# Kernel optimization log

Hardware: AMD Instinct MI355X
Metric: run time of the kernel (lower is better)

Reference implementation:

```python
import jax, jax.numpy as jnp
import numpy as np

D_MODEL = 1024
NUM_HEADS = 16
DK = D_MODEL // NUM_HEADS
THETA = 10000.0
B, S = 4, 2048


def _rope(x, pos):
    # x: [B, H, S, dk], pos: [S] int positions
    half = DK // 2
    inv_freq = THETA ** (-jnp.arange(half, dtype=jnp.float32) * 2.0 / DK)  # [half]
    ang = pos.astype(jnp.float32)[:, None] * inv_freq[None, :]             # [S, half]
    cos, sin = jnp.cos(ang), jnp.sin(ang)                                  # [S, half]
    x_even = x[..., 0::2]
    x_odd = x[..., 1::2]
    out_even = x_even * cos - x_odd * sin
    out_odd = x_even * sin + x_odd * cos
    # interleave back to [..., dk]
    return jnp.stack([out_even, out_odd], axis=-1).reshape(x.shape)


def setup_inputs() -> dict:
    key = jax.random.key(0)
    ks = jax.random.split(key, 5)
    scale = 1.0 / np.sqrt(D_MODEL)
    return {
        "x": jax.random.normal(ks[0], (B, S, D_MODEL), dtype=jnp.float32),
        "token_position": jnp.arange(S, dtype=jnp.int32),
        "wq": jax.random.normal(ks[1], (D_MODEL, D_MODEL), dtype=jnp.float32) * scale,
        "wk": jax.random.normal(ks[2], (D_MODEL, D_MODEL), dtype=jnp.float32) * scale,
        "wv": jax.random.normal(ks[3], (D_MODEL, D_MODEL), dtype=jnp.float32) * scale,
        "wo": jax.random.normal(ks[4], (D_MODEL, D_MODEL), dtype=jnp.float32) * scale,
    }


def reference(x, token_position, wq, wk, wv, wo):
    b, s, _ = x.shape
    # QKV projections (torch Linear: y = x @ W.T), split heads -> [B, H, S, dk]
    def proj(w):
        y = jnp.einsum("bsd,ed->bse", x, w)
        return y.reshape(b, s, NUM_HEADS, DK).transpose(0, 2, 1, 3)
    q, k, v = proj(wq), proj(wk), proj(wv)
    q = _rope(q, token_position)
    k = _rope(k, token_position)
    # causal SDPA
    scores = jnp.einsum("bhqd,bhkd->bhqk", q, k) / jnp.sqrt(jnp.float32(DK))
    causal = jnp.tril(jnp.ones((s, s), dtype=bool))
    scores = jnp.where(causal, scores, -jnp.inf)
    attn = jax.nn.softmax(scores, axis=-1)
    out = jnp.einsum("bhqk,bhkd->bhqd", attn, v)          # [B, H, S, dv]
    out = out.transpose(0, 2, 1, 3).reshape(b, s, D_MODEL)  # merge heads
    return jnp.einsum("bsd,ed->bse", out, wo)             # output projection
```

## Files before the change

### kernel.cpp

```cpp
#include <hip/hip_runtime.h>


#define D_MODEL 1024
#define NH      16
#define DKH     64
#define SEQ     2048
#define BATCH   4
#define SCALE_LOG2 0.180336875461f
#define ROPE_L2    0.41524101186092029f

typedef _Float16 f16;
typedef _Float16 f16x8 __attribute__((ext_vector_type(8)));
typedef _Float16 f16x4 __attribute__((ext_vector_type(4)));
typedef __fp16   fp16x2n __attribute__((ext_vector_type(2)));
typedef float    f32x4 __attribute__((ext_vector_type(4)));
typedef unsigned short u16;
typedef unsigned int   u32;

__device__ __forceinline__ void glds16(const void* g, void* l) {
  __builtin_amdgcn_global_load_lds((const __attribute__((address_space(1))) void*)g,
                                   (__attribute__((address_space(3))) void*)l, 16, 0, 0);
}
__device__ __forceinline__ u32 pk(float a, float b) {
  union { fp16x2n h; u32 u; } c; c.h = __builtin_amdgcn_cvt_pkrtz(a, b); return c.u;
}

#define VMW_(N) asm volatile("s_waitcnt vmcnt(" #N ")" ::: "memory")
#define VMW(N) VMW_(N)
#define PRE_MFMA() do {                                                       \
    __builtin_amdgcn_s_barrier();                                             \
    asm volatile("s_waitcnt lgkmcnt(0)" ::: "memory");                        \
    __builtin_amdgcn_sched_barrier(0);                                        \
  } while (0)

__global__ void cvt_all(const float* __restrict__ x,
                        const float* __restrict__ w0, const float* __restrict__ w1,
                        const float* __restrict__ w2, const float* __restrict__ w3,
                        f16* __restrict__ xo, f16* __restrict__ o0, f16* __restrict__ o1,
                        f16* __restrict__ o2, f16* __restrict__ o3) {
  int blk = blockIdx.x;
  const float* src; f16* dst; int off;
  if (blk < 8192) { src = x; dst = xo; off = blk; }
  else {
    int t = blk - 8192; int w = t >> 10; off = t & 1023;
    switch (w) { case 0: src = w0; dst = o0; break;  case 1: src = w1; dst = o1; break;
                 case 2: src = w2; dst = o2; break;  default: src = w3; dst = o3; break; }
  }
  int i = (off * 256 + threadIdx.x) * 4;
  float4 v = *(const float4*)(src + i);
  uint2 o; o.x = pk(v.x, v.y); o.y = pk(v.z, v.w);
  *(uint2*)(dst + i) = o;
}

__global__ __launch_bounds__(512, 2) void gemm_qkv(const f16* __restrict__ A,
                                                   const f16* __restrict__ W,
                                                   f16* __restrict__ Qo,
                                                   f16* __restrict__ Ko,
                                                   f16* __restrict__ Vo,
                                                   const int* __restrict__ pos) {
  extern __shared__ char lds[];
  const int bid  = blockIdx.x;
  const int lin  = (bid & 7) * 64 + (bid >> 3);
  const int bx   = lin & 15, by = lin >> 4;
  const int m0   = by * 256, n0 = bx * 192;
  const int tid  = threadIdx.x;
  const int wave = tid >> 6, lane = tid & 63;
  const int quad = lane >> 4, l16 = lane & 15;
  const int wr   = wave >> 2, wc = wave & 3;

  f32x4 acc[8][3];
#pragma unroll
  for (int i = 0; i < 8; ++i)
#pragma unroll
    for (int j = 0; j < 3; ++j) acc[i][j] = (f32x4){0.f, 0.f, 0.f, 0.f};

  const int posR = (l16 & 1) * 4 + (quad ^ ((l16 >> 1) & 3));
  const char* aRd  = lds + wr * 8192 + (l16 >> 1) * 128 + posR * 16;
  const char* bRd0 = lds + 65536 + (wc * 48 + l16) * 128 + ((quad) ^ (l16 & 7)) * 16;
  const char* bRd1 = lds + 65536 + (wc * 48 + l16) * 128 + ((4 + quad) ^ (l16 & 7)) * 16;

  const int srA = tid >> 3;
  const int rA  = 2 * srA + ((tid >> 2) & 1);
  const int cA  = (tid & 3) ^ (srA & 3);
  const f16* pA0 = A + (size_t)(m0 + rA) * 1024 + cA * 8;
  const f16* pA1 = pA0 + (size_t)128 * 1024;
  const int gB = (tid & 7) ^ ((tid >> 3) & 7);
  const f16* pB0 = W + (size_t)(n0 + (tid >> 3)) * 1024 + gB * 8;
  const f16* pB1 = pB0 + (size_t)64 * 1024;
  const f16* pB2 = pB0 + (size_t)128 * 1024;
  char* const sdA = lds + (size_t)(tid & 448) * 16;
  char* const sdB = lds + 65536 + (size_t)(tid & 448) * 16;

#define ST_A(TB, H) do {                                                      \
    glds16(pA0 + (H) * 32, sdA + (TB) * 32768 + (H) * 16384);                 \
    glds16(pA1 + (H) * 32, sdA + (TB) * 32768 + (H) * 16384 + 8192);          \
  } while (0)
#define ST_B(TB) do {                                                         \
    glds16(pB0, sdB + (TB) * 24576);                                          \
    glds16(pB1, sdB + (TB) * 24576 + 8192);                                   \
    glds16(pB2, sdB + (TB) * 24576 + 16384);                                  \
  } while (0)
#define RDA(BUF, H, MG) do { _Pragma("unroll")                                \
    for (int i_ = 0; i_ < 4; ++i_)                                            \
      af[i_] = *(const f16x8*)(aRd + (BUF) * 32768 + (H) * 16384 +            \
                               (MG) * 4096 + i_ * 1024);                      \
  } while (0)
#define RDB(BUF, H) do { _Pragma("unroll")                                    \
    for (int j_ = 0; j_ < 3; ++j_)                                            \
      bf[j_] = *(const f16x8*)(((H) ? bRd1 : bRd0) + (BUF) * 24576 + j_ * 2048);\
  } while (0)
#define MMQ(MG) do {                                                          \
    __builtin_amdgcn_s_setprio(1);                                            \
    _Pragma("unroll")                                                         \
    for (int i_ = 0; i_ < 4; ++i_) { _Pragma("unroll")                        \
      for (int j_ = 0; j_ < 3; ++j_)                                          \
        acc[(MG) * 4 + i_][j_] = __builtin_amdgcn_mfma_f32_16x16x32_f16(      \
            af[i_], bf[j_], acc[(MG) * 4 + i_][j_], 0, 0, 0); }               \
    __builtin_amdgcn_s_setprio(0);                                            \
  } while (0)

#define TILE(BUF, DOSTAGE, VM2, LAST) do {                                    \
    f16x8 af[4]; f16x8 bf[3];                                                 \
    RDA(BUF, 0, 0); RDB(BUF, 0);                                              \
    if (DOSTAGE) ST_A((BUF) ^ 1, 0);                                          \
    PRE_MFMA(); MMQ(0);                                                       \
    __builtin_amdgcn_s_barrier();                                             \
    RDA(BUF, 0, 1);                                                           \
    if (DOSTAGE) ST_B((BUF) ^ 1);                                             \
    PRE_MFMA(); MMQ(1);                                                       \
    VMW(VM2); __builtin_amdgcn_sched_barrier(0);                              \
    __builtin_amdgcn_s_barrier();                                             \
    RDA(BUF, 1, 0); RDB(BUF, 1);                                              \
    if (DOSTAGE) ST_A((BUF) ^ 1, 1);                                          \
    PRE_MFMA(); MMQ(0);                                                       \
    __builtin_amdgcn_s_barrier();                                             \
    RDA(BUF, 1, 1);                                                           \
    PRE_MFMA(); MMQ(1);                                                       \
    if (!(LAST)) {                                                            \
      VMW_(2); __builtin_amdgcn_sched_barrier(0);                             \
      __builtin_amdgcn_s_barrier();                                           \
    }                                                                         \
    if (DOSTAGE) { pA0 += 64; pA1 += 64; pB0 += 64; pB1 += 64; pB2 += 64; }   \
  } while (0)

  ST_A(0, 0); ST_B(0); ST_A(0, 1);
  pA0 += 64; pA1 += 64; pB0 += 64; pB1 += 64; pB2 += 64;
  VMW_(2); __builtin_amdgcn_sched_barrier(0);
  __builtin_amdgcn_s_barrier();

#pragma unroll 1
  for (int it = 0; it < 7; ++it) {
    TILE(0, 1, 5, 0);
    TILE(1, 1, 5, 0);
  }
  TILE(0, 1, 5, 0);
  TILE(1, 0, 0, 1);

#undef TILE
#undef MMQ
#undef RDB
#undef RDA
#undef ST_B
#undef ST_A

  f16* dsts[3]; int colB[3]; bool rp[3]; float invf[3], sgn[3];
#pragma unroll
  for (int ni = 0; ni < 3; ++ni) {
    int gc  = n0 + wc * 48 + ni * 16 + l16;
    int seg = gc >> 10;
    dsts[ni] = (seg == 0) ? Qo : (seg == 1) ? Ko : Vo;
    colB[ni] = gc & 1023;
    rp[ni]   = (seg < 2);
    int dk   = gc & 63;
    invf[ni] = __builtin_amdgcn_exp2f(-ROPE_L2 * (float)(dk >> 1));
    sgn[ni]  = (dk & 1) ? 1.f : -1.f;
  }
#pragma unroll
  for (int a = 0; a < 8; ++a)
#pragma unroll
    for (int r = 0; r < 4; ++r) {
      int row = m0 + wr * 128 + a * 16 + quad * 4 + r;
      float ps = (float)pos[row & (SEQ - 1)];
#pragma unroll
      for (int ni = 0; ni < 3; ++ni) {
        float v = acc[a][ni][r];
        float ov;
        if (rp[ni]) {
          float ang = ps * invf[ni];
          float c = __cosf(ang), sn = __sinf(ang);
          float p = __shfl_xor(v, 1);
          ov = fmaf(p * sgn[ni], sn, v * c);
        } else ov = v;
        dsts[ni][(size_t)row * 1024 + colB[ni]] = (f16)ov;
      }
    }
}

__global__ __launch_bounds__(512, 2) void gemm_out(const f16* __restrict__ A,
                                                   const f16* __restrict__ W,
                                                   float* __restrict__ C) {
  extern __shared__ char lds[];
  const int bid  = blockIdx.x;
  const int lin  = (bid & 7) * 32 + (bid >> 3);
  const int bx   = lin & 3, by = lin >> 2;
  const int m0   = by * 128, n0 = bx * 256;
  const int tid  = threadIdx.x;
  const int wave = tid >> 6, lane = tid & 63;
  const int quad = lane >> 4, l16 = lane & 15;
  const int wr   = wave >> 2, wc = wave & 3;

  f32x4 acc[4][4];
#pragma unroll
  for (int i = 0; i < 4; ++i)
#pragma unroll
    for (int j = 0; j < 4; ++j) acc[i][j] = (f32x4){0.f, 0.f, 0.f, 0.f};

  const int posR = (l16 & 1) * 4 + (quad ^ ((l16 >> 1) & 3));
  const char* aRd = lds + wr * 4096 + (l16 >> 1) * 128 + posR * 16;
  const char* bRd = lds + 32768 + wc * 4096 + (l16 >> 1) * 128 + posR * 16;

  const int srA = tid >> 3;
  const int rA  = 2 * srA + ((tid >> 2) & 1);
  const int cA  = (tid & 3) ^ (srA & 3);
  const f16* pA = A + (size_t)(m0 + rA) * 1024 + cA * 8;
  const int rB  = 2 * (tid >> 3) + ((tid >> 2) & 1);
  const int cB  = (tid & 3) ^ ((tid >> 3) & 3);
  const f16* pB0 = W + (size_t)(n0 + rB) * 1024 + cB * 8;
  const f16* pB1 = pB0 + (size_t)128 * 1024;
  char* const sdA = lds + (size_t)(tid & 448) * 16;
  char* const sdB = lds + 32768 + (size_t)(tid & 448) * 16;

#define ST_AO(TB, H) glds16(pA + (H) * 32, sdA + (TB) * 16384 + (H) * 8192)
#define ST_BO(TB, H) do {                                                     \
    glds16(pB0 + (H) * 32, sdB + (TB) * 32768 + (H) * 16384);                 \
    glds16(pB1 + (H) * 32, sdB + (TB) * 32768 + (H) * 16384 + 8192);          \
  } while (0)
#define HALF(BUF, H, DOSTAGE, VMN, LAST) do {                                 \
    f16x8 af[4], bf[4];                                                       \
    _Pragma("unroll")                                                         \
    for (int i_ = 0; i_ < 4; ++i_)                                            \
      af[i_] = *(const f16x8*)(aRd + (BUF) * 16384 + (H) * 8192 + i_ * 1024); \
    _Pragma("unroll")                                                         \
    for (int j_ = 0; j_ < 4; ++j_)                                            \
      bf[j_] = *(const f16x8*)(bRd + (BUF) * 32768 + (H) * 16384 + j_ * 1024);\
    if (DOSTAGE) { ST_AO((BUF) ^ 1, H); ST_BO((BUF) ^ 1, H); }                \
    PRE_MFMA();                                                               \
    __builtin_amdgcn_s_setprio(1);                                            \
    _Pragma("unroll")                                                         \
    for (int i_ = 0; i_ < 4; ++i_) { _Pragma("unroll")                        \
      for (int j_ = 0; j_ < 4; ++j_)                                          \
        acc[i_][j_] = __builtin_amdgcn_mfma_f32_16x16x32_f16(                 \
            af[i_], bf[j_], acc[i_][j_], 0, 0, 0); }                          \
    __builtin_amdgcn_s_setprio(0);                                            \
    if (!(LAST)) {                                                            \
      VMW(VMN); __builtin_amdgcn_sched_barrier(0);                            \
      __builtin_amdgcn_s_barrier();                                           \
    }                                                                         \
  } while (0)

  ST_AO(0, 0); ST_BO(0, 0); ST_AO(0, 1); ST_BO(0, 1);
  pA += 64; pB0 += 64; pB1 += 64;
  VMW_(3); __builtin_amdgcn_sched_barrier(0);
  __builtin_amdgcn_s_barrier();

#pragma unroll 1
  for (int it = 0; it < 7; ++it) {
    HALF(0, 0, 1, 3, 0); HALF(0, 1, 1, 3, 0); pA += 64; pB0 += 64; pB1 += 64;
    HALF(1, 0, 1, 3, 0); HALF(1, 1, 1, 3, 0); pA += 64; pB0 += 64; pB1 += 64;
  }
  HALF(0, 0, 1, 3, 0); HALF(0, 1, 1, 3, 0);
  HALF(1, 0, 0, 0, 0);
  HALF(1, 1, 0, 0, 1);

#undef HALF
#undef ST_BO
#undef ST_AO

  float* dst = C;
#pragma unroll
  for (int a = 0; a < 4; ++a)
#pragma unroll
    for (int ni = 0; ni < 4; ++ni)
#pragma unroll
      for (int r = 0; r < 4; ++r) {
        int row = m0 + wr * 64 + a * 16 + quad * 4 + r;
        int col = n0 + wc * 64 + ni * 16 + l16;
        dst[(size_t)row * 1024 + col] = acc[a][ni][r];
      }
}

__global__ __launch_bounds__(256, 3) void flash_attn(const f16* __restrict__ Q,
                                                     const f16* __restrict__ Kg,
                                                     const f16* __restrict__ Vg,
                                                     f16* __restrict__ O) {
  __shared__ char smem[38400];
  f16*  KsL         = (f16*)smem;
  u32   (*Vt)[67]   = (u32(*)[67])(smem + 16384);
  float (*Red0)[66] = (float(*)[66])smem;
  float (*Red1)[66] = (float(*)[66])(smem + 16896);
  float (*Lb)[17]   = (float(*)[17])(smem + 33792);

  const int tid  = threadIdx.x;
  const int bh   = blockIdx.x;
  const int b    = bh >> 4, h = bh & 15;
  const int qblk = 31 - (int)blockIdx.y;
  const int q0   = qblk * 64;
  const int wave = tid >> 6, lane = tid & 63;
  const int quad = lane >> 4, l16 = lane & 15;
  const int nkt  = (qblk + 2) >> 1;

  f16x8 qf[4][2];
#pragma unroll
  for (int nt = 0; nt < 4; ++nt)
#pragma unroll
    for (int ks = 0; ks < 2; ++ks) {
      f16x8 qv = *(const f16x8*)(Q + ((size_t)(b * SEQ + q0 + nt * 16 + l16)) * D_MODEL
                                   + h * DKH + ks * 32 + quad * 8);
      qf[nt][ks] = qv * (f16)SCALE_LOG2;
    }

  f32x4 o[4][4];
#pragma unroll
  for (int md = 0; md < 4; ++md)
#pragma unroll
    for (int nt = 0; nt < 4; ++nt) o[md][nt] = (f32x4){0.f, 0.f, 0.f, 0.f};
  float lacc[4] = {0.f, 0.f, 0.f, 0.f};

  const int kp = tid >> 3, dc = (tid & 7) * 8;

  for (int t = 0; t < nkt; ++t) {
    const int kt = t * 128;
    const f16* vb = Vg + ((size_t)(b * SEQ + kt + 2 * kp)) * D_MODEL + h * DKH + dc;
    uint4 v0 = *(const uint4*)vb;
    uint4 v1 = *(const uint4*)(vb + D_MODEL);
    uint4 v2 = *(const uint4*)(vb + 64 * D_MODEL);
    uint4 v3 = *(const uint4*)(vb + 65 * D_MODEL);

    if (t) __syncthreads();
#pragma unroll
    for (int i = 0; i < 4; ++i) {
      int ci = i * 256 + tid;
      int row = ci >> 3, gc = (ci & 7) ^ (row & 7);
      glds16(Kg + ((size_t)(b * SEQ + kt + row)) * D_MODEL + h * DKH + gc * 8,
             smem + (size_t)(i * 256 + (tid & 192)) * 16);
    }
    {
      union { uint4 u; u16 s[8]; } a0, a1, a2, a3;
      a0.u = v0; a1.u = v1; a2.u = v2; a3.u = v3;
#pragma unroll
      for (int j = 0; j < 8; ++j) {
        Vt[dc + j][kp]      = (u32)a0.s[j] | ((u32)a1.s[j] << 16);
        Vt[dc + j][32 + kp] = (u32)a2.s[j] | ((u32)a3.s[j] << 16);
      }
    }
    __syncthreads();

    f16x4 pb[2][4];
#pragma unroll
    for (int mt = 0; mt < 2; ++mt) {
      const int krow = wave * 32 + mt * 16 + l16;
      const int s0 = quad ^ (krow & 7);
      f16x8 ka0 = *(const f16x8*)(KsL + krow * 64 + s0 * 8);
      f16x8 ka1 = *(const f16x8*)(KsL + krow * 64 + (s0 ^ 4) * 8);
      const int keyb = kt + wave * 32 + mt * 16 + quad * 4;
#pragma unroll
      for (int nt = 0; nt < 4; ++nt) {
        f32x4 c = (f32x4){0.f, 0.f, 0.f, 0.f};
        c = __builtin_amdgcn_mfma_f32_16x16x32_f16(ka0, qf[nt][0], c, 0, 0, 0);
        c = __builtin_amdgcn_mfma_f32_16x16x32_f16(ka1, qf[nt][1], c, 0, 0, 0);
        const int q = q0 + nt * 16 + l16;
        float p0 = __builtin_amdgcn_exp2f(c[0]);
        float p1 = __builtin_amdgcn_exp2f(c[1]);
        float p2 = __builtin_amdgcn_exp2f(c[2]);
        float p3 = __builtin_amdgcn_exp2f(c[3]);
        if (t == nkt - 1) {
          p0 = (keyb + 0 <= q) ? p0 : 0.f;
          p1 = (keyb + 1 <= q) ? p1 : 0.f;
          p2 = (keyb + 2 <= q) ? p2 : 0.f;
          p3 = (keyb + 3 <= q) ? p3 : 0.f;
        }
        lacc[nt] += (p0 + p1) + (p2 + p3);
        union { u32 w[2]; f16x4 v; } pp;
        pp.w[0] = pk(p0, p1); pp.w[1] = pk(p2, p3);
        pb[mt][nt] = pp.v;
      }
    }

#pragma unroll
    for (int md = 0; md < 4; ++md)
#pragma unroll
      for (int ks2 = 0; ks2 < 2; ++ks2) {
        const u32* vp = &Vt[md * 16 + l16][wave * 16 + ks2 * 8 + quad * 2];
        union { u32 x[2]; f16x4 v; } va;
        va.x[0] = vp[0]; va.x[1] = vp[1];
#pragma unroll
        for (int nt = 0; nt < 4; ++nt)
          o[md][nt] = __builtin_amdgcn_mfma_f32_16x16x16f16(va.v, pb[ks2][nt], o[md][nt], 0, 0, 0);
      }
  }

  __syncthreads();
  {
    float (*Rw)[66] = (wave >= 2) ? Red1 : Red0;
    if ((wave & 1) == 0) {
#pragma unroll
      for (int md = 0; md < 4; ++md)
#pragma unroll
        for (int nt = 0; nt < 4; ++nt)
#pragma unroll
          for (int r = 0; r < 4; ++r)
            Rw[md * 16 + quad * 4 + r][nt * 16 + l16] = o[md][nt][r];
    }
#pragma unroll
    for (int nt = 0; nt < 4; ++nt)
      Lb[nt * 16 + l16][wave * 4 + quad] = lacc[nt];
    __syncthreads();
    if (wave & 1) {
#pragma unroll
      for (int md = 0; md < 4; ++md)
#pragma unroll
        for (int nt = 0; nt < 4; ++nt)
#pragma unroll
          for (int r = 0; r < 4; ++r)
            Rw[md * 16 + quad * 4 + r][nt * 16 + l16] += o[md][nt][r];
    }
    __syncthreads();
  }

  {
    const int q = tid & 63, dc4 = (tid >> 6) * 16;
    float lsum = 0.f;
#pragma unroll
    for (int j = 0; j < 16; ++j) lsum += Lb[q][j];
    float linv = __builtin_amdgcn_rcpf(lsum);
    union { uint4 u[2]; u32 w[8]; } ov;
#pragma unroll
    for (int i = 0; i < 8; ++i) {
      float f0 = Red0[dc4 + 2 * i][q]     + Red1[dc4 + 2 * i][q];
      float f1 = Red0[dc4 + 2 * i + 1][q] + Red1[dc4 + 2 * i + 1][q];
      ov.w[i] = pk(f0 * linv, f1 * linv);
    }
    f16* op = O + ((size_t)(b * SEQ + q0 + q)) * D_MODEL + h * DKH + dc4;
    *(uint4*)op = ov.u[0];
    *(uint4*)(op + 8) = ov.u[1];
  }
}

extern "C" void kernel_launch(void* const* d_in, const int* in_sizes, int n_in,
                              void* d_out, int out_size, void* d_ws, size_t ws_size,
                              hipStream_t stream) {
  const float* x      = (const float*)d_in[0];
  const int*   tokpos = (const int*)d_in[1];
  const float* wq     = (const float*)d_in[2];
  const float* wk     = (const float*)d_in[3];
  const float* wv     = (const float*)d_in[4];
  const float* wo     = (const float*)d_in[5];
  float* out = (float*)d_out;

  char* ws = (char*)d_ws;
  f16* Xb  = (f16*)(ws + 0);
  f16* Wqb = (f16*)(ws + 16777216);
  f16* Wkb = (f16*)(ws + 18874368);
  f16* Wvb = (f16*)(ws + 20971520);
  f16* Wob = (f16*)(ws + 23068672);
  f16* Qb  = (f16*)(ws + 25165824);
  f16* Kb  = (f16*)(ws + 41943040);
  f16* Vb  = (f16*)(ws + 58720256);
  f16* Ob  = Xb;

  static bool attr_done = false;
  if (!attr_done) {
    (void)hipFuncSetAttribute(reinterpret_cast<const void*>(gemm_qkv),
                              hipFuncAttributeMaxDynamicSharedMemorySize, 114688);
    (void)hipFuncSetAttribute(reinterpret_cast<const void*>(gemm_out),
                              hipFuncAttributeMaxDynamicSharedMemorySize, 98304);
    attr_done = true;
  }

  cvt_all<<<12288, 256, 0, stream>>>(x, wq, wk, wv, wo, Xb, Wqb, Wkb, Wvb, Wob);

  gemm_qkv<<<512, 512, 114688, stream>>>(Xb, Wqb, Qb, Kb, Vb, tokpos);

  flash_attn<<<dim3(BATCH * NH, 32), 256, 0, stream>>>(Qb, Kb, Vb, Ob);

  gemm_out<<<256, 512, 98304, stream>>>(Ob, Wob, out);
}
```

Before: 246.6 us.

## Double-buffer GEMM register fragments to overlap LDS reads with MFMA

Restructures the QKV projection GEMM main loop so A/B fragments are held in two register sets. The next quarter-tile's fragments, including the first fragments of the next LDS buffer, are read from LDS while MFMAs run on the current set. This drops the per-quarter barrier plus lgkmcnt(0) waits before every MFMA group, retunes the vmcnt waits, and peels the last tile into an epilogue. The extra fragment registers raise register pressure. Removing explicit sched barriers also leaves more of the instruction ordering to the compiler.

Result: no change. 246.9 us (+0.1%).

```diff
diff --git a/kernel.cpp b/kernel.cpp
--- a/kernel.cpp
+++ b/kernel.cpp
@@ -27,6 +27,7 @@
 
 #define VMW_(N) asm volatile("s_waitcnt vmcnt(" #N ")" ::: "memory")
 #define VMW(N) VMW_(N)
+#define BAR() __builtin_amdgcn_s_barrier()
 #define PRE_MFMA() do {                                                       \
     __builtin_amdgcn_s_barrier();                                             \
     asm volatile("s_waitcnt lgkmcnt(0)" ::: "memory");                        \
@@ -91,6 +92,9 @@
   char* const sdA = lds + (size_t)(tid & 448) * 16;
   char* const sdB = lds + 65536 + (size_t)(tid & 448) * 16;
 
+  f16x8 af[2][4];
+  f16x8 bf[2][3];
+
 #define ST_A(TB, H) do {                                                      \
     glds16(pA0 + (H) * 32, sdA + (TB) * 32768 + (H) * 16384);                 \
     glds16(pA1 + (H) * 32, sdA + (TB) * 32768 + (H) * 16384 + 8192);          \
@@ -100,66 +104,71 @@
     glds16(pB1, sdB + (TB) * 24576 + 8192);                                   \
     glds16(pB2, sdB + (TB) * 24576 + 16384);                                  \
   } while (0)
-#define RDA(BUF, H, MG) do { _Pragma("unroll")                                \
+#define RDAF(S, BUF, H, MG) do { _Pragma("unroll")                            \
     for (int i_ = 0; i_ < 4; ++i_)                                            \
-      af[i_] = *(const f16x8*)(aRd + (BUF) * 32768 + (H) * 16384 +            \
-                               (MG) * 4096 + i_ * 1024);                      \
-  } while (0)
-#define RDB(BUF, H) do { _Pragma("unroll")                                    \
+      af[S][i_] = *(const f16x8*)(aRd + (BUF) * 32768 + (H) * 16384 +         \
+                                  (MG) * 4096 + i_ * 1024);                   \
+  } while (0)
+#define RDBF(S, BUF, H) do { _Pragma("unroll")                                \
     for (int j_ = 0; j_ < 3; ++j_)                                            \
-      bf[j_] = *(const f16x8*)(((H) ? bRd1 : bRd0) + (BUF) * 24576 + j_ * 2048);\
-  } while (0)
-#define MMQ(MG) do {                                                          \
+      bf[S][j_] = *(const f16x8*)(((H) ? bRd1 : bRd0) + (BUF) * 24576 +       \
+                                  j_ * 2048);                                 \
+  } while (0)
+#define MMQ(AS, BS, MG) do {                                                  \
     __builtin_amdgcn_s_setprio(1);                                            \
     _Pragma("unroll")                                                         \
     for (int i_ = 0; i_ < 4; ++i_) { _Pragma("unroll")                        \
       for (int j_ = 0; j_ < 3; ++j_)                                          \
         acc[(MG) * 4 + i_][j_] = __builtin_amdgcn_mfma_f32_16x16x32_f16(      \
-            af[i_], bf[j_], acc[(MG) * 4 + i_][j_], 0, 0, 0); }               \
+            af[AS][i_], bf[BS][j_], acc[(MG) * 4 + i_][j_], 0, 0, 0); }       \
     __builtin_amdgcn_s_setprio(0);                                            \
   } while (0)
 
-#define TILE(BUF, DOSTAGE, VM2, LAST) do {                                    \
-    f16x8 af[4]; f16x8 bf[3];                                                 \
-    RDA(BUF, 0, 0); RDB(BUF, 0);                                              \
-    if (DOSTAGE) ST_A((BUF) ^ 1, 0);                                          \
-    PRE_MFMA(); MMQ(0);                                                       \
-    __builtin_amdgcn_s_barrier();                                             \
-    RDA(BUF, 0, 1);                                                           \
-    if (DOSTAGE) ST_B((BUF) ^ 1);                                             \
-    PRE_MFMA(); MMQ(1);                                                       \
-    VMW(VM2); __builtin_amdgcn_sched_barrier(0);                              \
-    __builtin_amdgcn_s_barrier();                                             \
-    RDA(BUF, 1, 0); RDB(BUF, 1);                                              \
-    if (DOSTAGE) ST_A((BUF) ^ 1, 1);                                          \
-    PRE_MFMA(); MMQ(0);                                                       \
-    __builtin_amdgcn_s_barrier();                                             \
-    RDA(BUF, 1, 1);                                                           \
-    PRE_MFMA(); MMQ(1);                                                       \
-    if (!(LAST)) {                                                            \
-      VMW_(2); __builtin_amdgcn_sched_barrier(0);                             \
-      __builtin_amdgcn_s_barrier();                                           \
-    }                                                                         \
-    if (DOSTAGE) { pA0 += 64; pA1 += 64; pB0 += 64; pB1 += 64; pB2 += 64; }   \
+#define TILEQ(BUF, DS, V1, V3) do {                                           \
+    RDAF(1, BUF, 0, 1);                                                       \
+    if (DS) ST_A((BUF) ^ 1, 0);                                               \
+    MMQ(0, 0, 0);                                                             \
+    VMW(V1); BAR();                                                           \
+    RDAF(0, BUF, 1, 0); RDBF(1, BUF, 1);                                      \
+    if (DS) ST_B((BUF) ^ 1);                                                  \
+    MMQ(1, 0, 1);                                                             \
+    BAR();                                                                    \
+    RDAF(1, BUF, 1, 1);                                                       \
+    if (DS) ST_A((BUF) ^ 1, 1);                                               \
+    MMQ(0, 1, 0);                                                             \
+    VMW(V3); BAR();                                                           \
+    RDAF(0, (BUF) ^ 1, 0, 0); RDBF(0, (BUF) ^ 1, 0);                          \
+    MMQ(1, 1, 1);                                                             \
+    if (DS) { pA0 += 64; pA1 += 64; pB0 += 64; pB1 += 64; pB2 += 64; }        \
   } while (0)
 
   ST_A(0, 0); ST_B(0); ST_A(0, 1);
   pA0 += 64; pA1 += 64; pB0 += 64; pB1 += 64; pB2 += 64;
-  VMW_(2); __builtin_amdgcn_sched_barrier(0);
-  __builtin_amdgcn_s_barrier();
+  VMW_(2);
+  BAR();
+  RDAF(0, 0, 0, 0);
+  RDBF(0, 0, 0);
 
 #pragma unroll 1
   for (int it = 0; it < 7; ++it) {
-    TILE(0, 1, 5, 0);
-    TILE(1, 1, 5, 0);
-  }
-  TILE(0, 1, 5, 0);
-  TILE(1, 0, 0, 1);
-
-#undef TILE
+    TILEQ(0, 1, 2, 2);
+    TILEQ(1, 1, 2, 2);
+  }
+  TILEQ(0, 1, 2, 2);
+
+  RDAF(1, 1, 0, 1);
+  MMQ(0, 0, 0);
+  VMW_(0); BAR();
+  RDAF(0, 1, 1, 0); RDBF(1, 1, 1);
+  MMQ(1, 0, 1);
+  RDAF(1, 1, 1, 1);
+  MMQ(0, 1, 0);
+  MMQ(1, 1, 1);
+
+#undef TILEQ
 #undef MMQ
-#undef RDB
-#undef RDA
+#undef RDBF
+#undef RDAF
 #undef ST_B
 #undef ST_A
 
```
